# Kernel tuning notes

Hardware: AMD Instinct MI355X
Metric: run time of the kernel (lower is better)

## Reference

```python
import jax, jax.numpy as jnp
from jax import lax
import numpy as np

K_SIZE = 3  # SteerableKernelBase.create_radial(3)


def _radial_basis_3x3():
    """Orthonormal radial steerable basis on a 3x3 grid.
    Returns 6 unit-norm kernels: [k0_center, k0_ring, k1_cos, k1_sin, k2_cos, k2_sin]."""
    ys, xs = np.mgrid[-1:2, -1:2].astype(np.float32)
    ang = np.arctan2(ys, xs)
    ring = (np.hypot(xs, ys) > 0).astype(np.float32)

    def unit(k):
        return (k / np.linalg.norm(k)).astype(np.float32)

    b0c = np.zeros((3, 3), np.float32); b0c[1, 1] = 1.0
    basis = np.stack([
        b0c,                       # k=0, r=0
        unit(ring),                # k=0, r=1
        unit(np.cos(ang) * ring),  # k=1 real
        unit(np.sin(ang) * ring),  # k=1 imag
        unit(np.cos(2 * ang) * ring),  # k=2 real
        unit(np.sin(2 * ang) * ring),  # k=2 imag
    ])
    return jnp.asarray(basis)  # (6, 3, 3)


def setup_inputs() -> dict:
    key = jax.random.key(0)
    k1, k2, k3 = jax.random.split(key, 3)
    N, C_in, C_out, H, W = 16, 64, 64, 128, 128
    x = jax.random.normal(k1, (N, C_in, H, W), dtype=jnp.float32)
    # steering angle field in [0,1); alpha = (cos 2*pi*theta, sin 2*pi*theta) is unitary
    theta = jax.random.uniform(k2, (N, 1, H, W), dtype=jnp.float32)
    # steerable weights: (n_out, n_in, 4) -> [k0 center, k0 ring, k1, k2]
    fan_in = C_in * K_SIZE * K_SIZE
    std = jnp.sqrt(2.0 / fan_in)  # relu gain init as in steerable_base.init_weights
    weights = jax.random.normal(k3, (C_out, C_in, 4), dtype=jnp.float32) * std
    bias = jnp.zeros((C_out,), dtype=jnp.float32)
    return {"x": x, "theta": theta, "weights": weights, "bias": bias}


def reference(x, theta, weights, bias):
    basis = _radial_basis_3x3()  # (6,3,3)
    O = weights.shape[0]
    w = weights[..., None, None]  # (O,I,4,1,1)
    # Synthesize per-harmonic kernels (O,I,3,3) from the steerable basis
    k0 = w[:, :, 0] * basis[0] + w[:, :, 1] * basis[1]
    k1r = w[:, :, 2] * basis[2]
    k1i = w[:, :, 2] * basis[3]
    k2r = w[:, :, 3] * basis[4]
    k2i = w[:, :, 3] * basis[5]
    ker = jnp.concatenate([k0, k1r, k1i, k2r, k2i], axis=0)  # (5O, I, 3, 3)

    z = lax.conv_general_dilated(
        x, ker, window_strides=(1, 1), padding="SAME",
        dimension_numbers=("NCHW", "OIHW", "NCHW"))  # (N, 5O, H, W)
    N, _, H, W = z.shape
    z = z.reshape(N, 5, O, H, W)

    # angle harmonics cos(k*alpha), sin(k*alpha); alpha unitary so rho=1 path
    a = 2.0 * jnp.pi * theta  # (N,1,H,W)
    c1, s1 = jnp.cos(a), jnp.sin(a)
    c2 = 2.0 * c1 * c1 - 1.0
    s2 = 2.0 * s1 * c1

    out = (z[:, 0] + c1 * z[:, 1] + s1 * z[:, 2]
           + c2 * z[:, 3] + s2 * z[:, 4])
    return out + bias[None, :, None, None]
```

## Files before the change

kernel.cpp:

```cpp
#include <hip/hip_runtime.h>


typedef __bf16 bf16x8 __attribute__((ext_vector_type(8)));
typedef float  f32x16 __attribute__((ext_vector_type(16)));
typedef float  f32x4  __attribute__((ext_vector_type(4)));
typedef float  f32x2  __attribute__((ext_vector_type(2)));
typedef unsigned int u32;
typedef const __attribute__((address_space(1))) u32* gp_t;
typedef __attribute__((address_space(3))) u32* lp_t;

#define HH 128
#define WW 128
#define HW 16384
#define CHIMG 65536

__device__ __forceinline__ f32x2 sp(float v) { return (f32x2){v, v}; }

__global__ void wt_repack(const float* __restrict__ wt,
                          unsigned short* __restrict__ wb) {
    int i = blockIdx.x * 256 + threadIdx.x;
    int o = i >> 8, k = i & 255;
    const float sc[4] = {1.f, 0.35355339059327373f, 0.35355339059327373f, 0.5f};
    union { float f; u32 u; } v; v.f = wt[i] * sc[k & 3];
    unsigned short b = (unsigned short)((v.u + 0x7FFF + ((v.u >> 16) & 1)) >> 16);
    int kcg = k >> 4, hxx = (k >> 3) & 1, r = k & 7;
    wb[((kcg * 2 + hxx) * 64 + o) * 8 + r] = b;
}

__global__ __launch_bounds__(256, 3) void steered_conv_mfma(
    const float* __restrict__ x, const float* __restrict__ theta,
    const unsigned short* __restrict__ wb, const float* __restrict__ bias,
    float* __restrict__ out)
{
    __shared__ __attribute__((aligned(16))) float xs[4][3][8][4][40];

    const int tid  = threadIdx.x;
    const int W    = tid >> 6;
    const int lane = tid & 63;
    const int pc = lane & 31, hx = lane >> 5;

    const int bb   = blockIdx.x;
    const int swz  = (bb & 7) * 128 + (bb >> 3);
    const int unit = swz * 4 + W;
    const int n    = unit >> 8;
    const int rem  = unit & 255;
    const int hA   = (rem >> 2) * 2;
    const int w0   = (rem & 3) * 32;
    const int w    = w0 + pc;

    int soff[5];
    #pragma unroll
    for (int d = 0; d < 5; ++d) {
        const int i   = d * 1024 + lane * 16;
        const int ch  = i / 640;
        const int rm  = i - ch * 640;
        const int row = rm / 160;
        const int c16 = rm - row * 160;
        const int gh  = hA - 1 + row;
        const int ghc = gh < 0 ? 0 : (gh > 127 ? 127 : gh);
        int so = ch * CHIMG + ghc * 512 + w0 * 4 - 16 + c16;
        so = so < 0 ? 0 : so;
        const bool sk = (gh < 0) | (gh > 127) |
                        ((w0 == 0) & (c16 < 16)) | ((w0 == 96) & (c16 >= 144));
        soff[d] = sk ? -1 : so;
    }

    const char* xn = (const char*)x + (size_t)n * 64 * CHIMG;

    float s1a, c1a, s1b, c1b;
    __sincosf(6.2831853071795864769f * theta[(n*HH + hA)*WW + w], &s1a, &c1a);
    __sincosf(6.2831853071795864769f * theta[(n*HH + hA+1)*WW + w], &s1b, &c1b);
    const float c2a = 2.f*c1a*c1a - 1.f, s2a = 2.f*s1a*c1a;
    const float c2b = 2.f*c1b*c1b - 1.f, s2b = 2.f*s1b*c1b;

    if (hA == 0 || hA == 126 || w0 == 0 || w0 == 96) {
        f32x4* z = (f32x4*)&xs[W][0][0][0][0];
        #pragma unroll
        for (int i = 0; i < 15; ++i)
            z[lane + i * 64] = f32x4{0.f, 0.f, 0.f, 0.f};
        asm volatile("s_waitcnt lgkmcnt(0)" ::: "memory");
    }

    auto stage = [&](int t) {
        const char* sb = xn + (size_t)(t * 8) * CHIMG;
        char* db = (char*)&xs[W][t % 3][0][0][0];
        #pragma unroll
        for (int d = 0; d < 5; ++d)
            if (soff[d] >= 0)
                __builtin_amdgcn_global_load_lds((gp_t)(sb + soff[d]),
                                                 (lp_t)(db + d * 1024), 16, 0, 0);
    };

    const unsigned short* wbl = wb + (hx * 64 + pc) * 8;
    bf16x8 wE0, wE1, wE2, wE3, wO0, wO1, wO2, wO3;

    stage(0);
    __builtin_amdgcn_sched_barrier(0);
    {
        const unsigned short* wr = wbl;
        wE0 = *(const bf16x8*)(wr);
        wE1 = *(const bf16x8*)(wr + 256);
        wE2 = *(const bf16x8*)(wr + 1024);
        wE3 = *(const bf16x8*)(wr + 1280);
    }
    __builtin_amdgcn_sched_barrier(0);
    stage(1);
    __builtin_amdgcn_sched_barrier(0);

    f32x16 acc00, acc01, acc10, acc11;
    #pragma unroll
    for (int r = 0; r < 16; ++r) { acc00[r]=0.f; acc01[r]=0.f; acc10[r]=0.f; acc11[r]=0.f; }

    #pragma unroll
    for (int c = 0; c < 8; ++c) {
        if (c == 7) asm volatile("s_waitcnt vmcnt(0)" ::: "memory");
        else        asm volatile("s_waitcnt vmcnt(5)" ::: "memory");
        __builtin_amdgcn_sched_barrier(0);
        if (c < 7) {
            const unsigned short* wr = wbl + (c + 1) * 2048;
            if ((c + 1) & 1) {
                wO0 = *(const bf16x8*)(wr);
                wO1 = *(const bf16x8*)(wr + 256);
                wO2 = *(const bf16x8*)(wr + 1024);
                wO3 = *(const bf16x8*)(wr + 1280);
            } else {
                wE0 = *(const bf16x8*)(wr);
                wE1 = *(const bf16x8*)(wr + 256);
                wE2 = *(const bf16x8*)(wr + 1024);
                wE3 = *(const bf16x8*)(wr + 1280);
            }
            __builtin_amdgcn_sched_barrier(0);
        }
        if (c < 6) {
            asm volatile("s_waitcnt lgkmcnt(0)" ::: "memory");
            __builtin_amdgcn_sched_barrier(0);
            stage(c + 2);
            __builtin_amdgcn_sched_barrier(0);
        }

        const bf16x8 A00 = (c & 1) ? wO0 : wE0;
        const bf16x8 A01 = (c & 1) ? wO1 : wE1;
        const bf16x8 A10 = (c & 1) ? wO2 : wE2;
        const bf16x8 A11 = (c & 1) ? wO3 : wE3;

        const float* tb = &xs[W][c % 3][0][0][0];
        #pragma unroll
        for (int kc = 0; kc < 2; ++kc) {
            const float* t = tb + (kc * 4 + hx * 2) * 160 + pc + 3;
            #define PAIR(off) (f32x2){t[off], t[(off) + 160]}
            const f32x2 L0 = PAIR(0),   Cc0 = PAIR(1),   R0 = PAIR(2);
            const f32x2 L1 = PAIR(40),  Cc1 = PAIR(41),  R1 = PAIR(42);
            const f32x2 L2 = PAIR(80),  Cc2 = PAIR(81),  R2 = PAIR(82);
            const f32x2 L3 = PAIR(120), Cc3 = PAIR(121), R3 = PAIR(122);
            #undef PAIR
            const f32x2 S0 = L0 + Cc0 + R0, S1 = L1 + Cc1 + R1;
            const f32x2 S2 = L2 + Cc2 + R2, S3 = L3 + Cc3 + R3;
            const f32x2 D0 = R0 - L0, D1 = R1 - L1;
            const f32x2 D2 = R2 - L2, D3 = R3 - L3;

            bf16x8 b0, b1;
            {
                const f32x2 T  = S1 - Cc1;
                const f32x2 F1 = S0 + S2 + T;
                const f32x2 B2 = (D0 + D2) + sp(1.4142135623730951f) * D1;
                const f32x2 B3 = (S2 - S0) + sp(0.4142135623730951f) * (Cc2 - Cc0);
                const f32x2 B4 = T - (Cc0 + Cc2);
                const f32x2 B5 = D2 - D0;
                const f32x2 F2 = sp(c1a) * B2 + sp(s1a) * B3;
                const f32x2 F3 = sp(c2a) * B4 + sp(s2a) * B5;
                b0[0]=(__bf16)Cc1.x; b0[1]=(__bf16)F1.x; b0[2]=(__bf16)F2.x; b0[3]=(__bf16)F3.x;
                b0[4]=(__bf16)Cc1.y; b0[5]=(__bf16)F1.y; b0[6]=(__bf16)F2.y; b0[7]=(__bf16)F3.y;
            }
            {
                const f32x2 T  = S2 - Cc2;
                const f32x2 F1 = S1 + S3 + T;
                const f32x2 B2 = (D1 + D3) + sp(1.4142135623730951f) * D2;
                const f32x2 B3 = (S3 - S1) + sp(0.4142135623730951f) * (Cc3 - Cc1);
                const f32x2 B4 = T - (Cc1 + Cc3);
                const f32x2 B5 = D3 - D1;
                const f32x2 F2 = sp(c1b) * B2 + sp(s1b) * B3;
                const f32x2 F3 = sp(c2b) * B4 + sp(s2b) * B5;
                b1[0]=(__bf16)Cc2.x; b1[1]=(__bf16)F1.x; b1[2]=(__bf16)F2.x; b1[3]=(__bf16)F3.x;
                b1[4]=(__bf16)Cc2.y; b1[5]=(__bf16)F1.y; b1[6]=(__bf16)F2.y; b1[7]=(__bf16)F3.y;
            }
            const bf16x8 A0 = kc ? A10 : A00;
            const bf16x8 A1 = kc ? A11 : A01;
            __builtin_amdgcn_s_setprio(1);
            acc00 = __builtin_amdgcn_mfma_f32_32x32x16_bf16(A0, b0, acc00, 0, 0, 0);
            acc01 = __builtin_amdgcn_mfma_f32_32x32x16_bf16(A1, b0, acc01, 0, 0, 0);
            acc10 = __builtin_amdgcn_mfma_f32_32x32x16_bf16(A0, b1, acc10, 0, 0, 0);
            acc11 = __builtin_amdgcn_mfma_f32_32x32x16_bf16(A1, b1, acc11, 0, 0, 0);
            __builtin_amdgcn_s_setprio(0);
        }
        __builtin_amdgcn_sched_barrier(0);
    }

    const size_t hw = (size_t)HW;
    float* op = out + (size_t)n * 64 * hw + (size_t)hA * WW + w;
    #pragma unroll
    for (int r = 0; r < 16; ++r) {
        const int o = (r & 3) + 8 * (r >> 2) + 4 * hx;
        const float bo = bias[o], bo2 = bias[o + 32];
        op[(size_t)o * hw]             = acc00[r] + bo;
        op[(size_t)(o + 32) * hw]      = acc01[r] + bo2;
        op[(size_t)o * hw + WW]        = acc10[r] + bo;
        op[(size_t)(o + 32) * hw + WW] = acc11[r] + bo2;
    }
}

extern "C" void kernel_launch(void* const* d_in, const int* in_sizes, int n_in,
                              void* d_out, int out_size, void* d_ws, size_t ws_size,
                              hipStream_t stream) {
    const float* x     = (const float*)d_in[0];
    const float* theta = (const float*)d_in[1];
    const float* wt    = (const float*)d_in[2];
    const float* bias  = (const float*)d_in[3];
    float* out = (float*)d_out;
    unsigned short* wb = (unsigned short*)d_ws;

    wt_repack<<<64, 256, 0, stream>>>(wt, wb);

    steered_conv_mfma<<<1024, 256, 0, stream>>>(x, theta, wb, bias, out);
}
```

Measured before the change: 38.46 us.

## Double-buffer LDS staging and transpose epilogue through LDS for vectorized stores

Cuts the per-wave LDS input staging from three buffers to two and moves the prefetch of the next chunk to after the MFMA compute, so the buffer being overwritten is no longer being read. The epilogue now writes each accumulator tile into LDS and reads it back transposed, so each lane issues 16-byte stores of consecutive pixels instead of scalar strided stores. Bias is loaded once as vectors up front. The smaller LDS footprint may allow higher occupancy, at the cost of less prefetch distance and extra LDS round trips and waits in the epilogue.

```diff
diff --git a/kernel.cpp b/kernel.cpp
--- a/kernel.cpp
+++ b/kernel.cpp
@@ -32,7 +32,7 @@
     const unsigned short* __restrict__ wb, const float* __restrict__ bias,
     float* __restrict__ out)
 {
-    __shared__ __attribute__((aligned(16))) float xs[4][3][8][4][40];
+    __shared__ __attribute__((aligned(16))) float xs[4][2][8][4][40];
 
     const int tid  = threadIdx.x;
     const int W    = tid >> 6;
@@ -47,6 +47,11 @@
     const int hA   = (rem >> 2) * 2;
     const int w0   = (rem & 3) * 32;
     const int w    = w0 + pc;
+
+    const int olp0 = (lane >> 3) * 4;
+    const f32x4 b4lo = *(const f32x4*)(bias + olp0);
+    const f32x4 b4hi = *(const f32x4*)(bias + 32 + olp0);
+    __builtin_amdgcn_sched_barrier(0);
 
     int soff[5];
     #pragma unroll
@@ -76,14 +81,14 @@
     if (hA == 0 || hA == 126 || w0 == 0 || w0 == 96) {
         f32x4* z = (f32x4*)&xs[W][0][0][0][0];
         #pragma unroll
-        for (int i = 0; i < 15; ++i)
+        for (int i = 0; i < 10; ++i)
             z[lane + i * 64] = f32x4{0.f, 0.f, 0.f, 0.f};
         asm volatile("s_waitcnt lgkmcnt(0)" ::: "memory");
     }
 
     auto stage = [&](int t) {
         const char* sb = xn + (size_t)(t * 8) * CHIMG;
-        char* db = (char*)&xs[W][t % 3][0][0][0];
+        char* db = (char*)&xs[W][t & 1][0][0][0];
         #pragma unroll
         for (int d = 0; d < 5; ++d)
             if (soff[d] >= 0)
@@ -131,19 +136,13 @@
             }
             __builtin_amdgcn_sched_barrier(0);
         }
-        if (c < 6) {
-            asm volatile("s_waitcnt lgkmcnt(0)" ::: "memory");
-            __builtin_amdgcn_sched_barrier(0);
-            stage(c + 2);
-            __builtin_amdgcn_sched_barrier(0);
-        }
 
         const bf16x8 A00 = (c & 1) ? wO0 : wE0;
         const bf16x8 A01 = (c & 1) ? wO1 : wE1;
         const bf16x8 A10 = (c & 1) ? wO2 : wE2;
         const bf16x8 A11 = (c & 1) ? wO3 : wE3;
 
-        const float* tb = &xs[W][c % 3][0][0][0];
+        const float* tb = &xs[W][c & 1][0][0][0];
         #pragma unroll
         for (int kc = 0; kc < 2; ++kc) {
             const float* t = tb + (kc * 4 + hx * 2) * 160 + pc + 3;
@@ -192,19 +191,40 @@
             acc11 = __builtin_amdgcn_mfma_f32_32x32x16_bf16(A1, b1, acc11, 0, 0, 0);
             __builtin_amdgcn_s_setprio(0);
         }
-        __builtin_amdgcn_sched_barrier(0);
-    }
-
-    const size_t hw = (size_t)HW;
-    float* op = out + (size_t)n * 64 * hw + (size_t)hA * WW + w;
-    #pragma unroll
-    for (int r = 0; r < 16; ++r) {
-        const int o = (r & 3) + 8 * (r >> 2) + 4 * hx;
-        const float bo = bias[o], bo2 = bias[o + 32];
-        op[(size_t)o * hw]             = acc00[r] + bo;
-        op[(size_t)(o + 32) * hw]      = acc01[r] + bo2;
-        op[(size_t)o * hw + WW]        = acc10[r] + bo;
-        op[(size_t)(o + 32) * hw + WW] = acc11[r] + bo2;
+        asm volatile("s_waitcnt lgkmcnt(0)" ::: "memory");
+        __builtin_amdgcn_sched_barrier(0);
+        if (c < 6) stage(c + 2);
+        __builtin_amdgcn_sched_barrier(0);
+    }
+
+    asm volatile("s_waitcnt lgkmcnt(0)" ::: "memory");
+    __builtin_amdgcn_sched_barrier(0);
+    float* T = (float*)&xs[W][0][0][0][0];
+    float* onb = out + (size_t)n * 64 * HW + (size_t)hA * WW + w0;
+    const int wq = lane & 7;
+    #pragma unroll
+    for (int q = 0; q < 4; ++q) {
+        const f32x16 aq = (q == 0) ? acc00 : (q == 1) ? acc01
+                        : (q == 2) ? acc10 : acc11;
+        const int rsel  = q >> 1;
+        const int ohalf = (q & 1) * 32;
+        #pragma unroll
+        for (int r = 0; r < 16; ++r) {
+            const int ol = (r & 3) + 8 * (r >> 2) + 4 * hx;
+            T[ol * 32 + pc] = aq[r];
+        }
+        asm volatile("s_waitcnt lgkmcnt(0)" ::: "memory");
+        __builtin_amdgcn_sched_barrier(0);
+        #pragma unroll
+        for (int i = 0; i < 4; ++i) {
+            const int olp = olp0 + i;
+            f32x4 v = *(const f32x4*)&T[olp * 32 + wq * 4];
+            const float bo = (q & 1) ? b4hi[i] : b4lo[i];
+            v.x += bo; v.y += bo; v.z += bo; v.w += bo;
+            *(f32x4*)(onb + (size_t)(ohalf + olp) * HW + rsel * WW + wq * 4) = v;
+        }
+        asm volatile("s_waitcnt lgkmcnt(0)" ::: "memory");
+        __builtin_amdgcn_sched_barrier(0);
     }
 }
 
```

Result: slower. 48.00 us (+24.8%).
